# Kernel optimization log

Hardware: AMD Instinct MI355X
Metric: run time of the kernel (lower is better)

## Reference

```python
import jax, jax.numpy as jnp
import numpy as np

MIN_RANGE = -128.0
MAX_RANGE = 127.0


def quantize(t, min_range=MIN_RANGE, max_range=MAX_RANGE):
    """Per-tensor affine (asymmetric) quantization, as in QuantizedMatrix.
    Returns (q, scale, zero_point) with q in [min_range, max_range]."""
    mn = jnp.min(t)
    mx = jnp.max(t)
    scale = (mx - mn) / (max_range - min_range)
    zero_point = jnp.round(min_range - mn / scale)
    q = jnp.clip(jnp.round(t / scale) + zero_point, min_range, max_range)
    return q, scale, zero_point


def setup_inputs() -> dict:
    key = jax.random.key(0)
    k1, k2, k3 = jax.random.split(key, 3)
    B, S, D_IN, D_OUT = 4, 2048, 4096, 4096
    x = jax.random.normal(k1, (B, S, D_IN), dtype=jnp.float32)
    # nn.Linear weight layout: [out_features, in_features]
    W = jax.random.normal(k2, (D_OUT, D_IN), dtype=jnp.float32) * (1.0 / np.sqrt(D_IN))
    bias = jax.random.normal(k3, (D_OUT,), dtype=jnp.float32) * 0.02
    return {"x": x, "W": W, "bias": bias}


def reference(x, W, bias):
    # Quantize activations (per-tensor over the whole [B,S,D] tensor) and weights.
    qx, sx, zx = quantize(x)
    qw, sw, zw = quantize(W)
    # QuantizedMatrix matmul: dequantized product
    #   s_x * s_w * (q_x - z_x) @ (q_w - z_w)^T  , W is [out,in] so contract on 'd'.
    acc = jnp.einsum("bsd,od->bso", qx - zx, qw - zw)
    res = (sx * sw) * acc + bias
    return res
```

## Files before the change

kernel.cpp:

```cpp
#include <hip/hip_runtime.h>

#define GM 8192
#define GN 4096
#define GK 4096
#define NT (GK / 64)

#define QX_OFF   0ull
#define QW_OFF   33554432ull
#define RSX_OFF  50331648ull
#define RSW_OFF  50364416ull
#define PRM_OFF  50380832ull

#define MMB_X 2048
#define MMB_W 1024

using v4i  = __attribute__((ext_vector_type(4)))  int;
using v16i = __attribute__((ext_vector_type(16))) int;

__device__ __forceinline__ unsigned encf(float x) {
    unsigned u = __float_as_uint(x);
    return (u & 0x80000000u) ? ~u : (u | 0x80000000u);
}
__device__ __forceinline__ float decf(unsigned e) {
    unsigned u = (e & 0x80000000u) ? (e & 0x7FFFFFFFu) : ~e;
    return __uint_as_float(u);
}

__device__ __forceinline__ void async16(const signed char* g, signed char* l) {
    __builtin_amdgcn_global_load_lds((const __attribute__((address_space(1))) void*)g,
                                     (__attribute__((address_space(3))) void*)l,
                                     16, 0, 0);
}

__global__ void k_minmax(const float4* __restrict__ x, const float4* __restrict__ Wt,
                         unsigned* __restrict__ part) {
    const float4* p; int n4, b0, nb; unsigned* dst;
    if (blockIdx.x < MMB_X) { p = x;  n4 = GM * GK / 4; b0 = blockIdx.x;         nb = MMB_X; dst = part;        }
    else                    { p = Wt; n4 = GN * GK / 4; b0 = blockIdx.x - MMB_X; nb = MMB_W; dst = part + 4096; }
    unsigned mx = 0u, nm = 0u;
    for (int i = b0 * 256 + threadIdx.x; i < n4; i += nb * 256) {
        float4 v = p[i];
        mx = max(mx, encf(v.x)); nm = max(nm, encf(-v.x));
        mx = max(mx, encf(v.y)); nm = max(nm, encf(-v.y));
        mx = max(mx, encf(v.z)); nm = max(nm, encf(-v.z));
        mx = max(mx, encf(v.w)); nm = max(nm, encf(-v.w));
    }
    #pragma unroll
    for (int o = 32; o > 0; o >>= 1) {
        mx = max(mx, (unsigned)__shfl_down((int)mx, o));
        nm = max(nm, (unsigned)__shfl_down((int)nm, o));
    }
    __shared__ unsigned smx[4], snm[4];
    int w = threadIdx.x >> 6;
    if ((threadIdx.x & 63) == 0) { smx[w] = mx; snm[w] = nm; }
    __syncthreads();
    if (threadIdx.x == 0) {
        #pragma unroll
        for (int i = 1; i < 4; i++) { mx = max(mx, smx[i]); nm = max(nm, snm[i]); }
        dst[b0]      = mx;
        dst[nb + b0] = nm;
    }
}

__global__ void k_params(const unsigned* __restrict__ part, float* prm) {
    const int t = threadIdx.x;
    unsigned v0 = 0u, v1 = 0u, v2 = 0u, v3 = 0u;
    for (int i = t; i < MMB_X; i += 256) {
        v0 = max(v0, part[i]);
        v1 = max(v1, part[MMB_X + i]);
    }
    for (int i = t; i < MMB_W; i += 256) {
        v2 = max(v2, part[4096 + i]);
        v3 = max(v3, part[5120 + i]);
    }
    #pragma unroll
    for (int o = 32; o > 0; o >>= 1) {
        v0 = max(v0, (unsigned)__shfl_down((int)v0, o));
        v1 = max(v1, (unsigned)__shfl_down((int)v1, o));
        v2 = max(v2, (unsigned)__shfl_down((int)v2, o));
        v3 = max(v3, (unsigned)__shfl_down((int)v3, o));
    }
    __shared__ unsigned s[4][4];
    const int wv = t >> 6;
    if ((t & 63) == 0) { s[wv][0] = v0; s[wv][1] = v1; s[wv][2] = v2; s[wv][3] = v3; }
    __syncthreads();
    if (t == 0) {
        #pragma unroll
        for (int i = 1; i < 4; i++) {
            v0 = max(v0, s[i][0]); v1 = max(v1, s[i][1]);
            v2 = max(v2, s[i][2]); v3 = max(v3, s[i][3]);
        }
        float mxx = decf(v0), mnx = -decf(v1);
        float sx  = (mxx - mnx) / 255.0f;
        float zxf = rintf(-128.0f - mnx / sx);
        float mxw = decf(v2), mnw = -decf(v3);
        float sw  = (mxw - mnw) / 255.0f;
        float zwf = rintf(-128.0f - mnw / sw);
        prm[0] = sx; prm[1] = zxf; prm[2] = sw; prm[3] = zwf; prm[4] = sx * sw;
        int* ip = (int*)prm;
        ip[5] = (int)zxf; ip[6] = (int)zwf;
    }
}

__global__ void k_quant(const float* __restrict__ x, const float* __restrict__ Wt,
                        signed char* __restrict__ qx, signed char* __restrict__ qw,
                        int* __restrict__ rsx, int* __restrict__ rsw,
                        const float* __restrict__ prm) {
    const float* src; signed char* q; int* rs; int pidx, row;
    if (blockIdx.x < GM) { row = blockIdx.x;      src = x;  q = qx; rs = rsx; pidx = 0; }
    else                 { row = blockIdx.x - GM; src = Wt; q = qw; rs = rsw; pidx = 2; }
    const int t = threadIdx.x;
    const float s  = prm[pidx];
    const float zp = prm[pidx + 1];
    const float4* srow = (const float4*)(src + (size_t)row * GK);
    int* qrow = (int*)(q + (size_t)row * GK);
    int acc = 0;
    #pragma unroll
    for (int i = 0; i < 4; i++) {
        float4 v = srow[i * 256 + t];
        int q0 = (int)fminf(fmaxf(rintf(v.x / s) + zp, -128.0f), 127.0f);
        int q1 = (int)fminf(fmaxf(rintf(v.y / s) + zp, -128.0f), 127.0f);
        int q2 = (int)fminf(fmaxf(rintf(v.z / s) + zp, -128.0f), 127.0f);
        int q3 = (int)fminf(fmaxf(rintf(v.w / s) + zp, -128.0f), 127.0f);
        acc += q0 + q1 + q2 + q3;
        qrow[i * 256 + t] = (q0 & 255) | ((q1 & 255) << 8) | ((q2 & 255) << 16)
                          | ((q3 & 255) << 24);
    }
    #pragma unroll
    for (int o = 32; o > 0; o >>= 1) acc += __shfl_down(acc, o);
    __shared__ int sa[4];
    if ((t & 63) == 0) sa[t >> 6] = acc;
    __syncthreads();
    if (t == 0) rs[row] = sa[0] + sa[1] + sa[2] + sa[3];
}

__global__ __launch_bounds__(512, 2) void k_gemm(
    const signed char* __restrict__ qx, const signed char* __restrict__ qw,
    const int* __restrict__ rsx, const int* __restrict__ rsw,
    const float* __restrict__ bias, const float* __restrict__ prm,
    float* __restrict__ out) {
    __shared__ __align__(16) signed char lds[3][2][256 * 64];

    const int tid  = threadIdx.x;
    const int lane = tid & 63;
    const int w    = tid >> 6;
    const int bid  = blockIdx.x;
    const int tm0  = (bid >> 4) * 256;
    const int tn0  = (bid & 15) * 256;

    const int slab = w & 3;
    const int sr   = lane >> 2;
    const int sc   = ((lane & 3) ^ ((lane >> 3) & 3)) * 16;
    const signed char* gsrc = (w < 4)
        ? qx + (size_t)(tm0 + slab * 64 + sr) * GK + sc
        : qw + (size_t)(tn0 + slab * 64 + sr) * GK + sc;
    const int ldsTensor = (w < 4) ? 0 : 1;
    const int ldsSlab   = slab * 64 * 64;

    const int wr = w >> 2;
    const int wc = w & 3;
    const int fr = lane & 31;
    const int fh = lane >> 5;

    v16i acc[4][2] = {};

    auto compute = [&](int rdi) {
        const signed char* cA = lds[rdi][0];
        const signed char* cB = lds[rdi][1];
        #pragma unroll
        for (int s = 0; s < 2; s++) {
            const int cc = s * 2 + fh;
            const int ca = (cc ^ ((fr >> 1) & 3)) * 16;
            v4i a0 = *(const v4i*)(cA + (wr * 128      + fr) * 64 + ca);
            v4i a1 = *(const v4i*)(cA + (wr * 128 + 32 + fr) * 64 + ca);
            v4i a2 = *(const v4i*)(cA + (wr * 128 + 64 + fr) * 64 + ca);
            v4i a3 = *(const v4i*)(cA + (wr * 128 + 96 + fr) * 64 + ca);
            v4i b0 = *(const v4i*)(cB + (wc * 64       + fr) * 64 + ca);
            v4i b1 = *(const v4i*)(cB + (wc * 64  + 32 + fr) * 64 + ca);
            acc[0][0] = __builtin_amdgcn_mfma_i32_32x32x32_i8(a0, b0, acc[0][0], 0, 0, 0);
            acc[0][1] = __builtin_amdgcn_mfma_i32_32x32x32_i8(a0, b1, acc[0][1], 0, 0, 0);
            acc[1][0] = __builtin_amdgcn_mfma_i32_32x32x32_i8(a1, b0, acc[1][0], 0, 0, 0);
            acc[1][1] = __builtin_amdgcn_mfma_i32_32x32x32_i8(a1, b1, acc[1][1], 0, 0, 0);
            acc[2][0] = __builtin_amdgcn_mfma_i32_32x32x32_i8(a2, b0, acc[2][0], 0, 0, 0);
            acc[2][1] = __builtin_amdgcn_mfma_i32_32x32x32_i8(a2, b1, acc[2][1], 0, 0, 0);
            acc[3][0] = __builtin_amdgcn_mfma_i32_32x32x32_i8(a3, b0, acc[3][0], 0, 0, 0);
            acc[3][1] = __builtin_amdgcn_mfma_i32_32x32x32_i8(a3, b1, acc[3][1], 0, 0, 0);
        }
    };

    #pragma unroll
    for (int j = 0; j < 4; j++)
        async16(gsrc + (size_t)j * 16 * GK, &lds[0][ldsTensor][ldsSlab + j * 1024]);
    #pragma unroll
    for (int j = 0; j < 4; j++)
        async16(gsrc + (size_t)j * 16 * GK + 64, &lds[1][ldsTensor][ldsSlab + j * 1024]);

    int rd = 0;
    for (int kt = 0; kt < NT - 2; ++kt) {
        asm volatile("s_waitcnt vmcnt(4)" ::: "memory");
        __builtin_amdgcn_s_barrier();
        asm volatile("" ::: "memory");
        int st = rd + 2; if (st >= 3) st -= 3;
        const size_t ko = (size_t)(kt + 2) * 64;
        #pragma unroll
        for (int j = 0; j < 4; j++)
            async16(gsrc + (size_t)j * 16 * GK + ko,
                    &lds[st][ldsTensor][ldsSlab + j * 1024]);
        compute(rd);
        rd = (rd + 1 == 3) ? 0 : rd + 1;
    }
    asm volatile("s_waitcnt vmcnt(4)" ::: "memory");
    __builtin_amdgcn_s_barrier();
    asm volatile("" ::: "memory");
    compute(rd);
    rd = (rd + 1 == 3) ? 0 : rd + 1;
    asm volatile("s_waitcnt vmcnt(0)" ::: "memory");
    __builtin_amdgcn_s_barrier();
    asm volatile("" ::: "memory");
    compute(rd);

    const float sxsw = prm[4];
    const int* ip = (const int*)prm;
    const int zxi = ip[5], zwi = ip[6];
    const int kzz = GK * zxi * zwi;
    #pragma unroll
    for (int i = 0; i < 4; i++) {
        #pragma unroll
        for (int j = 0; j < 2; j++) {
            const int col = tn0 + wc * 64 + j * 32 + fr;
            const int ccol = kzz - zxi * rsw[col];
            const float bv = bias[col];
            #pragma unroll
            for (int reg = 0; reg < 16; reg++) {
                const int row = tm0 + wr * 128 + i * 32
                              + (reg & 3) + 8 * (reg >> 2) + 4 * fh;
                const int t = acc[i][j][reg] - zwi * rsx[row] + ccol;
                out[(size_t)row * GN + col] = fmaf(sxsw, (float)t, bv);
            }
        }
    }
}

extern "C" void kernel_launch(void* const* d_in, const int* in_sizes, int n_in,
                              void* d_out, int out_size, void* d_ws, size_t ws_size,
                              hipStream_t stream) {
    const float* x    = (const float*)d_in[0];
    const float* Wt   = (const float*)d_in[1];
    const float* bias = (const float*)d_in[2];
    float* out = (float*)d_out;

    char* ws = (char*)d_ws;
    signed char* qx = (signed char*)(ws + QX_OFF);
    signed char* qw = (signed char*)(ws + QW_OFF);
    int* rsx = (int*)(ws + RSX_OFF);
    int* rsw = (int*)(ws + RSW_OFF);
    unsigned* part = (unsigned*)(ws + QX_OFF);
    float* prm = (float*)(ws + PRM_OFF);

    k_minmax<<<MMB_X + MMB_W, 256, 0, stream>>>((const float4*)x, (const float4*)Wt, part);
    k_params<<<1, 256, 0, stream>>>(part, prm);
    k_quant<<<GM + GN, 256, 0, stream>>>(x, Wt, qx, qw, rsx, rsw, prm);
    k_gemm<<<(GM / 256) * (GN / 256), 512, 0, stream>>>(qx, qw, rsx, rsw, bias,
                                                        prm, out);
}
```

Before: 440.7 us.

## Software-pipeline GEMM fragment loads, remap blocks, use float min/max reduction

The GEMM main loop now double-buffers LDS fragment reads into registers and overlaps them with MFMA issue, splitting each k-tile into two half-steps with barriers. Global-to-LDS loads are interleaved across the halves, and MFMA runs at raised wave priority. Block IDs are remapped so neighbouring blocks land on different XCDs for better L2 locality. The min/max pass switches from order-preserving integer encoding to plain float fmaxf/fminf, which drops a few ALU ops but doubles the barrier count per tile and adds more complex wait-count logic.

```diff
diff --git a/kernel.cpp b/kernel.cpp
--- a/kernel.cpp
+++ b/kernel.cpp
@@ -17,15 +17,6 @@
 using v4i  = __attribute__((ext_vector_type(4)))  int;
 using v16i = __attribute__((ext_vector_type(16))) int;
 
-__device__ __forceinline__ unsigned encf(float x) {
-    unsigned u = __float_as_uint(x);
-    return (u & 0x80000000u) ? ~u : (u | 0x80000000u);
-}
-__device__ __forceinline__ float decf(unsigned e) {
-    unsigned u = (e & 0x80000000u) ? (e & 0x7FFFFFFFu) : ~e;
-    return __uint_as_float(u);
-}
-
 __device__ __forceinline__ void async16(const signed char* g, signed char* l) {
     __builtin_amdgcn_global_load_lds((const __attribute__((address_space(1))) void*)g,
                                      (__attribute__((address_space(3))) void*)l,
@@ -33,69 +24,65 @@
 }
 
 __global__ void k_minmax(const float4* __restrict__ x, const float4* __restrict__ Wt,
-                         unsigned* __restrict__ part) {
-    const float4* p; int n4, b0, nb; unsigned* dst;
+                         float* __restrict__ part) {
+    const float4* p; int n4, b0, nb; float* dst;
     if (blockIdx.x < MMB_X) { p = x;  n4 = GM * GK / 4; b0 = blockIdx.x;         nb = MMB_X; dst = part;        }
     else                    { p = Wt; n4 = GN * GK / 4; b0 = blockIdx.x - MMB_X; nb = MMB_W; dst = part + 4096; }
-    unsigned mx = 0u, nm = 0u;
+    float mx = -3.4e38f, mn = 3.4e38f;
     for (int i = b0 * 256 + threadIdx.x; i < n4; i += nb * 256) {
         float4 v = p[i];
-        mx = max(mx, encf(v.x)); nm = max(nm, encf(-v.x));
-        mx = max(mx, encf(v.y)); nm = max(nm, encf(-v.y));
-        mx = max(mx, encf(v.z)); nm = max(nm, encf(-v.z));
-        mx = max(mx, encf(v.w)); nm = max(nm, encf(-v.w));
+        mx = fmaxf(mx, fmaxf(fmaxf(v.x, v.y), fmaxf(v.z, v.w)));
+        mn = fminf(mn, fminf(fminf(v.x, v.y), fminf(v.z, v.w)));
     }
     #pragma unroll
     for (int o = 32; o > 0; o >>= 1) {
-        mx = max(mx, (unsigned)__shfl_down((int)mx, o));
-        nm = max(nm, (unsigned)__shfl_down((int)nm, o));
-    }
-    __shared__ unsigned smx[4], snm[4];
+        mx = fmaxf(mx, __shfl_down(mx, o));
+        mn = fminf(mn, __shfl_down(mn, o));
+    }
+    __shared__ float smx[4], smn[4];
     int w = threadIdx.x >> 6;
-    if ((threadIdx.x & 63) == 0) { smx[w] = mx; snm[w] = nm; }
+    if ((threadIdx.x & 63) == 0) { smx[w] = mx; smn[w] = mn; }
     __syncthreads();
     if (threadIdx.x == 0) {
         #pragma unroll
-        for (int i = 1; i < 4; i++) { mx = max(mx, smx[i]); nm = max(nm, snm[i]); }
+        for (int i = 1; i < 4; i++) { mx = fmaxf(mx, smx[i]); mn = fminf(mn, smn[i]); }
         dst[b0]      = mx;
-        dst[nb + b0] = nm;
-    }
-}
-
-__global__ void k_params(const unsigned* __restrict__ part, float* prm) {
+        dst[nb + b0] = mn;
+    }
+}
+
+__global__ void k_params(const float* __restrict__ part, float* prm) {
     const int t = threadIdx.x;
-    unsigned v0 = 0u, v1 = 0u, v2 = 0u, v3 = 0u;
+    float v0 = -3.4e38f, v1 = 3.4e38f, v2 = -3.4e38f, v3 = 3.4e38f;
     for (int i = t; i < MMB_X; i += 256) {
-        v0 = max(v0, part[i]);
-        v1 = max(v1, part[MMB_X + i]);
+        v0 = fmaxf(v0, part[i]);
+        v1 = fminf(v1, part[MMB_X + i]);
     }
     for (int i = t; i < MMB_W; i += 256) {
-        v2 = max(v2, part[4096 + i]);
-        v3 = max(v3, part[5120 + i]);
+        v2 = fmaxf(v2, part[4096 + i]);
+        v3 = fminf(v3, part[5120 + i]);
     }
     #pragma unroll
     for (int o = 32; o > 0; o >>= 1) {
-        v0 = max(v0, (unsigned)__shfl_down((int)v0, o));
-        v1 = max(v1, (unsigned)__shfl_down((int)v1, o));
-        v2 = max(v2, (unsigned)__shfl_down((int)v2, o));
-        v3 = max(v3, (unsigned)__shfl_down((int)v3, o));
-    }
-    __shared__ unsigned s[4][4];
+        v0 = fmaxf(v0, __shfl_down(v0, o));
+        v1 = fminf(v1, __shfl_down(v1, o));
+        v2 = fmaxf(v2, __shfl_down(v2, o));
+        v3 = fminf(v3, __shfl_down(v3, o));
+    }
+    __shared__ float s[4][4];
     const int wv = t >> 6;
     if ((t & 63) == 0) { s[wv][0] = v0; s[wv][1] = v1; s[wv][2] = v2; s[wv][3] = v3; }
     __syncthreads();
     if (t == 0) {
         #pragma unroll
         for (int i = 1; i < 4; i++) {
-            v0 = max(v0, s[i][0]); v1 = max(v1, s[i][1]);
-            v2 = max(v2, s[i][2]); v3 = max(v3, s[i][3]);
-        }
-        float mxx = decf(v0), mnx = -decf(v1);
-        float sx  = (mxx - mnx) / 255.0f;
-        float zxf = rintf(-128.0f - mnx / sx);
-        float mxw = decf(v2), mnw = -decf(v3);
-        float sw  = (mxw - mnw) / 255.0f;
-        float zwf = rintf(-128.0f - mnw / sw);
+            v0 = fmaxf(v0, s[i][0]); v1 = fminf(v1, s[i][1]);
+            v2 = fmaxf(v2, s[i][2]); v3 = fminf(v3, s[i][3]);
+        }
+        float sx  = (v0 - v1) / 255.0f;
+        float zxf = rintf(-128.0f - v1 / sx);
+        float sw  = (v2 - v3) / 255.0f;
+        float zwf = rintf(-128.0f - v3 / sw);
         prm[0] = sx; prm[1] = zxf; prm[2] = sw; prm[3] = zwf; prm[4] = sx * sw;
         int* ip = (int*)prm;
         ip[5] = (int)zxf; ip[6] = (int)zwf;
@@ -144,7 +131,7 @@
     const int tid  = threadIdx.x;
     const int lane = tid & 63;
     const int w    = tid >> 6;
-    const int bid  = blockIdx.x;
+    const int bid  = ((blockIdx.x & 7) << 6) | (blockIdx.x >> 3);
     const int tm0  = (bid >> 4) * 256;
     const int tn0  = (bid & 15) * 256;
 
@@ -163,29 +150,31 @@
     const int fh = lane >> 5;
 
     v16i acc[4][2] = {};
-
-    auto compute = [&](int rdi) {
-        const signed char* cA = lds[rdi][0];
-        const signed char* cB = lds[rdi][1];
-        #pragma unroll
-        for (int s = 0; s < 2; s++) {
-            const int cc = s * 2 + fh;
-            const int ca = (cc ^ ((fr >> 1) & 3)) * 16;
-            v4i a0 = *(const v4i*)(cA + (wr * 128      + fr) * 64 + ca);
-            v4i a1 = *(const v4i*)(cA + (wr * 128 + 32 + fr) * 64 + ca);
-            v4i a2 = *(const v4i*)(cA + (wr * 128 + 64 + fr) * 64 + ca);
-            v4i a3 = *(const v4i*)(cA + (wr * 128 + 96 + fr) * 64 + ca);
-            v4i b0 = *(const v4i*)(cB + (wc * 64       + fr) * 64 + ca);
-            v4i b1 = *(const v4i*)(cB + (wc * 64  + 32 + fr) * 64 + ca);
-            acc[0][0] = __builtin_amdgcn_mfma_i32_32x32x32_i8(a0, b0, acc[0][0], 0, 0, 0);
-            acc[0][1] = __builtin_amdgcn_mfma_i32_32x32x32_i8(a0, b1, acc[0][1], 0, 0, 0);
-            acc[1][0] = __builtin_amdgcn_mfma_i32_32x32x32_i8(a1, b0, acc[1][0], 0, 0, 0);
-            acc[1][1] = __builtin_amdgcn_mfma_i32_32x32x32_i8(a1, b1, acc[1][1], 0, 0, 0);
-            acc[2][0] = __builtin_amdgcn_mfma_i32_32x32x32_i8(a2, b0, acc[2][0], 0, 0, 0);
-            acc[2][1] = __builtin_amdgcn_mfma_i32_32x32x32_i8(a2, b1, acc[2][1], 0, 0, 0);
-            acc[3][0] = __builtin_amdgcn_mfma_i32_32x32x32_i8(a3, b0, acc[3][0], 0, 0, 0);
-            acc[3][1] = __builtin_amdgcn_mfma_i32_32x32x32_i8(a3, b1, acc[3][1], 0, 0, 0);
-        }
+    v4i  fa[4], fb[2];
+
+    auto LDF = [&](int bi, int s) {
+        const signed char* cA = lds[bi][0];
+        const signed char* cB = lds[bi][1];
+        const int cc = s * 2 + fh;
+        const int ca = (cc ^ ((fr >> 1) & 3)) * 16;
+        fa[0] = *(const v4i*)(cA + (wr * 128      + fr) * 64 + ca);
+        fa[1] = *(const v4i*)(cA + (wr * 128 + 32 + fr) * 64 + ca);
+        fa[2] = *(const v4i*)(cA + (wr * 128 + 64 + fr) * 64 + ca);
+        fa[3] = *(const v4i*)(cA + (wr * 128 + 96 + fr) * 64 + ca);
+        fb[0] = *(const v4i*)(cB + (wc * 64       + fr) * 64 + ca);
+        fb[1] = *(const v4i*)(cB + (wc * 64  + 32 + fr) * 64 + ca);
+    };
+    auto MM = [&]() {
+        __builtin_amdgcn_s_setprio(1);
+        acc[0][0] = __builtin_amdgcn_mfma_i32_32x32x32_i8(fa[0], fb[0], acc[0][0], 0, 0, 0);
+        acc[0][1] = __builtin_amdgcn_mfma_i32_32x32x32_i8(fa[0], fb[1], acc[0][1], 0, 0, 0);
+        acc[1][0] = __builtin_amdgcn_mfma_i32_32x32x32_i8(fa[1], fb[0], acc[1][0], 0, 0, 0);
+        acc[1][1] = __builtin_amdgcn_mfma_i32_32x32x32_i8(fa[1], fb[1], acc[1][1], 0, 0, 0);
+        acc[2][0] = __builtin_amdgcn_mfma_i32_32x32x32_i8(fa[2], fb[0], acc[2][0], 0, 0, 0);
+        acc[2][1] = __builtin_amdgcn_mfma_i32_32x32x32_i8(fa[2], fb[1], acc[2][1], 0, 0, 0);
+        acc[3][0] = __builtin_amdgcn_mfma_i32_32x32x32_i8(fa[3], fb[0], acc[3][0], 0, 0, 0);
+        acc[3][1] = __builtin_amdgcn_mfma_i32_32x32x32_i8(fa[3], fb[1], acc[3][1], 0, 0, 0);
+        __builtin_amdgcn_s_setprio(0);
     };
 
     #pragma unroll
@@ -194,30 +183,39 @@
     #pragma unroll
     for (int j = 0; j < 4; j++)
         async16(gsrc + (size_t)j * 16 * GK + 64, &lds[1][ldsTensor][ldsSlab + j * 1024]);
-
-    int rd = 0;
-    for (int kt = 0; kt < NT - 2; ++kt) {
-        asm volatile("s_waitcnt vmcnt(4)" ::: "memory");
-        __builtin_amdgcn_s_barrier();
-        asm volatile("" ::: "memory");
-        int st = rd + 2; if (st >= 3) st -= 3;
-        const size_t ko = (size_t)(kt + 2) * 64;
-        #pragma unroll
-        for (int j = 0; j < 4; j++)
-            async16(gsrc + (size_t)j * 16 * GK + ko,
-                    &lds[st][ldsTensor][ldsSlab + j * 1024]);
-        compute(rd);
-        rd = (rd + 1 == 3) ? 0 : rd + 1;
-    }
     asm volatile("s_waitcnt vmcnt(4)" ::: "memory");
     __builtin_amdgcn_s_barrier();
-    asm volatile("" ::: "memory");
-    compute(rd);
-    rd = (rd + 1 == 3) ? 0 : rd + 1;
-    asm volatile("s_waitcnt vmcnt(0)" ::: "memory");
-    __builtin_amdgcn_s_barrier();
-    asm volatile("" ::: "memory");
-    compute(rd);
+    LDF(0, 0);
+
+    int rd = 0;
+    for (int kt = 0; kt < NT; ++kt) {
+        int st = rd + 2; if (st >= 3) st -= 3;
+        const int nrd = (rd + 1 == 3) ? 0 : rd + 1;
+        const size_t ko = (size_t)(kt + 2) * 64;
+        const bool stg = (kt < NT - 2);
+        __builtin_amdgcn_s_barrier();
+        asm volatile("s_waitcnt lgkmcnt(0)" ::: "memory");
+        __builtin_amdgcn_sched_barrier(0);
+        MM();
+        LDF(rd, 1);
+        if (stg) {
+            async16(gsrc + (size_t)0 * 16 * GK + ko, &lds[st][ldsTensor][ldsSlab + 0 * 1024]);
+            async16(gsrc + (size_t)1 * 16 * GK + ko, &lds[st][ldsTensor][ldsSlab + 1 * 1024]);
+            asm volatile("s_waitcnt vmcnt(2)" ::: "memory");
+        } else if (kt == NT - 2) {
+            asm volatile("s_waitcnt vmcnt(0)" ::: "memory");
+        }
+        __builtin_amdgcn_s_barrier();
+        asm volatile("s_waitcnt lgkmcnt(0)" ::: "memory");
+        __builtin_amdgcn_sched_barrier(0);
+        MM();
+        if (kt < NT - 1) LDF(nrd, 0);
+        if (stg) {
+            async16(gsrc + (size_t)2 * 16 * GK + ko, &lds[st][ldsTensor][ldsSlab + 2 * 1024]);
+            async16(gsrc + (size_t)3 * 16 * GK + ko, &lds[st][ldsTensor][ldsSlab + 3 * 1024]);
+        }
+        rd = nrd;
+    }
 
     const float sxsw = prm[4];
     const int* ip = (const int*)prm;
@@ -254,7 +252,7 @@
     signed char* qw = (signed char*)(ws + QW_OFF);
     int* rsx = (int*)(ws + RSX_OFF);
     int* rsw = (int*)(ws + RSW_OFF);
-    unsigned* part = (unsigned*)(ws + QX_OFF);
+    float* part = (float*)(ws + QX_OFF);
     float* prm = (float*)(ws + PRM_OFF);
 
     k_minmax<<<MMB_X + MMB_W, 256, 0, stream>>>((const float4*)x, (const float4*)Wt, part);
```

Measured after the change: 442.3 us. No clear change (+0.3%).
